# Kernel optimization log

Hardware: AMD Instinct MI355X
Metric: run time of the kernel (lower is better)

## Reference

```python
import jax, jax.numpy as jnp
import numpy as np

SIZE_VERTEX = 262144  # number of graph vertices (2**18)
D = 128               # embedding dim
B = 8192              # batch of (v_i, v_j) skip-gram pairs


def _build_leaf_map(n):
    # Faithful iterative version of build(): in-order leaf assignment of the
    # segment tree over [1, n+1]; leaf[k] = tree node id of the k-th leaf.
    leaf = np.zeros(n + 1, dtype=np.int64)
    stack = [(1, n + 1, 1)]
    while stack:
        tl, tr, v = stack.pop()
        if tl == tr:
            leaf[tl - 1] = v
        else:
            tm = (tl + tr) >> 1
            stack.append((tl, tm, 2 * v))
            stack.append((tm + 1, tr, 2 * v + 1))
    return leaf


def _build_paths(v_i, n):
    # path_root_v(leaf): nodes from child-of-root down to leaf (root excluded).
    # Step j uses weight row path[j] and sign +1 if path[j+1] == 2*path[j] else -1.
    leaf = _build_leaf_map(n)
    paths = []
    for node in leaf[np.asarray(v_i)]:
        p = []
        x = int(node)
        while x != 1:
            p.append(x)
            x //= 2
        paths.append(p[::-1])
    L = max(len(p) for p in paths) - 1  # number of sigmoid steps (padded)
    idx = np.zeros((len(paths), L), dtype=np.int32)
    sign = np.zeros((len(paths), L), dtype=np.int32)
    mask = np.zeros((len(paths), L), dtype=bool)
    for b, p in enumerate(paths):
        for j in range(len(p) - 1):
            idx[b, j] = p[j]
            sign[b, j] = 1 if p[j + 1] == 2 * p[j] else -1
            mask[b, j] = True
    return idx, sign, mask


def setup_inputs() -> dict:
    key = jax.random.key(0)
    k_enc, k_log, k_vi, k_vj = jax.random.split(key, 4)
    # torch.rand -> uniform [0, 1)
    encoder = jax.random.uniform(k_enc, (SIZE_VERTEX, D), dtype=jnp.float32)
    logistic = jax.random.uniform(k_log, (4 * SIZE_VERTEX, D), dtype=jnp.float32)
    v_i = np.asarray(jax.random.randint(k_vi, (B,), 0, SIZE_VERTEX))
    v_j = jax.random.randint(k_vj, (B,), 0, SIZE_VERTEX)
    path_idx, path_sign, path_mask = _build_paths(v_i, SIZE_VERTEX)
    return {
        "encoder": encoder,
        "logistic": logistic,
        "v_j": v_j,
        "path_idx": jnp.asarray(path_idx),
        "path_sign": jnp.asarray(path_sign),
        "path_mask": jnp.asarray(path_mask),
    }


def reference(encoder, logistic, v_j, path_idx, path_sign, path_mask):
    # one-hot mask @ encoder == direct row gather
    h = encoder[v_j]                                   # [B, D]
    w = logistic[path_idx]                             # [B, L, D]
    logits = jnp.einsum("bld,bd->bl", w, h)            # [B, L]
    logits = logits * path_sign.astype(h.dtype)
    probs = jnp.where(path_mask, jax.nn.sigmoid(logits), jnp.asarray(1.0, h.dtype))
    return jnp.prod(probs, axis=1)                     # [B]
```

## Files before the change

### kernel.cpp

```cpp
#include <hip/hip_runtime.h>
#include <hip/hip_bf16.h>


#define D 128

__global__ __launch_bounds__(256) void hs_prob_kernel(
    const float* __restrict__ encoder,
    const float* __restrict__ logistic,
    const int*   __restrict__ v_j,
    const int*   __restrict__ path_idx,
    const int*   __restrict__ path_sign,
    float*       __restrict__ out,
    int B, int L)
{
    const int gtid = blockIdx.x * blockDim.x + threadIdx.x;
    const int wave = gtid >> 6;
    const int lane = threadIdx.x & 63;
    if (wave >= B) return;
    const int b = wave;

    const int vj = v_j[b];
    const float2 h = ((const float2*)(encoder + (long long)vj * D))[lane];

    const int* idxp = path_idx  + (long long)b * L;
    const int* sgnp = path_sign + (long long)b * L;

    float prod = 1.0f;
    for (int l = 0; l < L; ++l) {
        const int sgn = sgnp[l];
        if (sgn == 0) break;
        const int idx = idxp[l];
        const float2 w = ((const float2*)(logistic + (long long)idx * D))[lane];

        float part = fmaf(w.x, h.x, w.y * h.y);
        #pragma unroll
        for (int off = 32; off; off >>= 1)
            part += __shfl_xor(part, off, 64);

        const float x = (float)sgn * part;
        prod *= 1.0f / (1.0f + expf(-x));
    }

    if (lane == 0) out[b] = prod;
}

extern "C" void kernel_launch(void* const* d_in, const int* in_sizes, int n_in,
                              void* d_out, int out_size, void* d_ws, size_t ws_size,
                              hipStream_t stream) {
    const float* encoder   = (const float*)d_in[0];
    const float* logistic  = (const float*)d_in[1];
    const int*   v_j       = (const int*)d_in[2];
    const int*   path_idx  = (const int*)d_in[3];
    const int*   path_sign = (const int*)d_in[4];

    const int B = in_sizes[2];
    const int L = in_sizes[3] / B;

    float* out = (float*)d_out;

    const int block = 256;
    const int grid  = (B * 64 + block - 1) / block;
    hipLaunchKernelGGL(hs_prob_kernel, dim3(grid), dim3(block), 0, stream,
                       encoder, logistic, v_j, path_idx, path_sign, out, B, L);
}
```

Measured before the change: 642.9 us.

## Split wave into half-waves processing two path steps each with float4 loads

Each wave now handles two path steps at once, one per 32-lane half-wave, using float4 loads of the weight row. The path indices and signs are loaded once into lanes, packed as signed indices, and broadcast by shuffle. The loop is unrolled by four to keep several independent gathers in flight, and expf is replaced with __expf. It aims to hide gather latency and remove the serialized per-step index loads and full 64-lane reductions, at the cost of more registers and a fast-math exponential. It assumes L is at most 64 and relies on the padded sign being zero to mask inactive steps.

After: 625.0 us. 1.03x faster.

```diff
diff --git a/kernel.cpp b/kernel.cpp
--- a/kernel.cpp
+++ b/kernel.cpp
@@ -19,27 +19,79 @@
     if (wave >= B) return;
     const int b = wave;
 
+    const int half    = lane >> 5;
+    const int sublane = lane & 31;
+
     const int vj = v_j[b];
-    const float2 h = ((const float2*)(encoder + (long long)vj * D))[lane];
+    const float4 h = ((const float4*)(encoder + (long long)vj * D))[sublane];
 
-    const int* idxp = path_idx  + (long long)b * L;
-    const int* sgnp = path_sign + (long long)b * L;
+    int c_l = 0;
+    if (lane < L)
+        c_l = path_sign[(long long)b * L + lane] * path_idx[(long long)b * L + lane];
 
+    const int S = (L + 2) >> 1;
     float prod = 1.0f;
-    for (int l = 0; l < L; ++l) {
-        const int sgn = sgnp[l];
-        if (sgn == 0) break;
-        const int idx = idxp[l];
-        const float2 w = ((const float2*)(logistic + (long long)idx * D))[lane];
 
-        float part = fmaf(w.x, h.x, w.y * h.y);
+    int s = 0;
+    for (; s + 4 <= S; s += 4) {
+        const int c0 = __shfl(c_l, 2*(s+0) + half, 64);
+        const int c1 = __shfl(c_l, 2*(s+1) + half, 64);
+        const int c2 = __shfl(c_l, 2*(s+2) + half, 64);
+        const int c3 = __shfl(c_l, 2*(s+3) + half, 64);
+
+        const int ix0 = c0 < 0 ? -c0 : c0;
+        const int ix1 = c1 < 0 ? -c1 : c1;
+        const int ix2 = c2 < 0 ? -c2 : c2;
+        const int ix3 = c3 < 0 ? -c3 : c3;
+
+        const float4 w0 = ((const float4*)(logistic + (long long)ix0 * D))[sublane];
+        const float4 w1 = ((const float4*)(logistic + (long long)ix1 * D))[sublane];
+        const float4 w2 = ((const float4*)(logistic + (long long)ix2 * D))[sublane];
+        const float4 w3 = ((const float4*)(logistic + (long long)ix3 * D))[sublane];
+
+        float p0 = fmaf(w0.x, h.x, fmaf(w0.y, h.y, fmaf(w0.z, h.z, w0.w * h.w)));
+        float p1 = fmaf(w1.x, h.x, fmaf(w1.y, h.y, fmaf(w1.z, h.z, w1.w * h.w)));
+        float p2 = fmaf(w2.x, h.x, fmaf(w2.y, h.y, fmaf(w2.z, h.z, w2.w * h.w)));
+        float p3 = fmaf(w3.x, h.x, fmaf(w3.y, h.y, fmaf(w3.z, h.z, w3.w * h.w)));
+
         #pragma unroll
-        for (int off = 32; off; off >>= 1)
-            part += __shfl_xor(part, off, 64);
+        for (int off = 16; off; off >>= 1) {
+            p0 += __shfl_xor(p0, off, 64);
+            p1 += __shfl_xor(p1, off, 64);
+            p2 += __shfl_xor(p2, off, 64);
+            p3 += __shfl_xor(p3, off, 64);
+        }
 
-        const float x = (float)sgn * part;
-        prod *= 1.0f / (1.0f + expf(-x));
+        const float x0 = c0 > 0 ? p0 : -p0;
+        const float x1 = c1 > 0 ? p1 : -p1;
+        const float x2 = c2 > 0 ? p2 : -p2;
+        const float x3 = c3 > 0 ? p3 : -p3;
+
+        const float f0 = 1.0f / (1.0f + __expf(-x0));
+        const float f1 = 1.0f / (1.0f + __expf(-x1));
+        const float f2 = 1.0f / (1.0f + __expf(-x2));
+        const float f3 = 1.0f / (1.0f + __expf(-x3));
+
+        prod *= (c0 ? f0 : 1.0f);
+        prod *= (c1 ? f1 : 1.0f);
+        prod *= (c2 ? f2 : 1.0f);
+        prod *= (c3 ? f3 : 1.0f);
     }
+
+    for (; s < S; ++s) {
+        const int c = __shfl(c_l, 2*s + half, 64);
+        const int ix = c < 0 ? -c : c;
+        const float4 w = ((const float4*)(logistic + (long long)ix * D))[sublane];
+        float p = fmaf(w.x, h.x, fmaf(w.y, h.y, fmaf(w.z, h.z, w.w * h.w)));
+        #pragma unroll
+        for (int off = 16; off; off >>= 1)
+            p += __shfl_xor(p, off, 64);
+        const float x = c > 0 ? p : -p;
+        const float f = 1.0f / (1.0f + __expf(-x));
+        prod *= (c ? f : 1.0f);
+    }
+
+    prod *= __shfl_xor(prod, 32, 64);
 
     if (lane == 0) out[b] = prod;
 }
```
